# Optimization experiments

Measured on AMD Instinct MI355X. Metric: run time of the kernel, lower is better.

## Reference

```python
import jax, jax.numpy as jnp
import numpy as np

B, N, H, HEADS = 8, 1024, 512, 4  # batch graphs, nodes/graph, graph_hsz, attention heads
R = 64  # relations per graph (passthrough)


def setup_inputs() -> dict:
    key = jax.random.key(0)
    k1, k2, k3, k4, k5, k6, k7 = jax.random.split(key, 7)
    adjs = jax.random.randint(k1, (B, N, N), 0, 2, dtype=jnp.int32)  # 0 => masked
    nodes = jax.random.normal(k2, (B, N, H), dtype=jnp.float32)
    triples = jax.random.normal(k3, (B, R, H), dtype=jnp.float32)   # unused in gat path
    relations = jax.random.normal(k4, (B, R, H), dtype=jnp.float32)  # passthrough
    node_num = jnp.full((B,), N, dtype=jnp.int32)  # all graphs full => no padding branch
    s = 1.0 / np.sqrt(H)
    Wq = (jax.random.normal(k5, (H, H), dtype=jnp.float32) * s)
    Wk = (jax.random.normal(k6, (H, H), dtype=jnp.float32) * s)
    Wv = (jax.random.normal(k7, (H, H), dtype=jnp.float32) * s)
    return {"adjs": adjs, "triples": triples, "nodes": nodes, "node_num": node_num,
            "relations": relations, "Wq": Wq, "Wk": Wk, "Wv": Wv}


def reference(adjs, triples, nodes, node_num, relations, Wq, Wk, Wv):
    b, n, h = nodes.shape
    dk = h // HEADS
    scale = 1.0 / jnp.sqrt(jnp.float32(h))  # torch divides by sqrt(key_dim)=sqrt(H)

    def to_heads(x, W):  # [B,N,H] -> [B,heads,N,dk]; matches split(dim=-1)+stack
        return (x @ W).reshape(b, n, HEADS, dk).transpose(0, 2, 1, 3)

    Q = to_heads(nodes, Wq)
    K = to_heads(nodes, Wk)
    V = to_heads(nodes, Wv)
    att = jnp.einsum('bhnd,bhmd->bhnm', Q, K) * scale
    att = jnp.where((adjs == 0)[:, None, :, :], -jnp.inf, att)
    p = jax.nn.softmax(att, axis=-1)  # dropout_p = blockdrop = 0.0 => identity
    out = jnp.einsum('bhnm,bhmd->bhnd', p, V)
    out = out.transpose(0, 2, 1, 3).reshape(b, n, h)  # concat heads along feature dim
    out = jax.nn.relu(out)
    return (out, relations)
```

## Files before the change

kernel.cpp:

```cpp
#include <hip/hip_runtime.h>
#include <stdint.h>

typedef __attribute__((ext_vector_type(4))) float f32x4;
typedef __attribute__((ext_vector_type(16))) float f32x16;
typedef __attribute__((ext_vector_type(8))) short bf16x8;
typedef __attribute__((ext_vector_type(4))) unsigned uint4v;
typedef unsigned long long ull;

#define GLB_AS const __attribute__((address_space(1)))
#define LDS_AS __attribute__((address_space(3)))

__device__ __forceinline__ short f2bf(float f) {
    union { float f; unsigned u; } x; x.f = f;
    unsigned r = x.u + 0x7FFFu + ((x.u >> 16) & 1u);
    return (short)(r >> 16);
}

__global__ void k_pre(const float* __restrict__ nodes, short* __restrict__ nodes_bf,
                      const float* __restrict__ Wq, const float* __restrict__ Wk,
                      const float* __restrict__ Wv, short* __restrict__ WT,
                      const int* __restrict__ adjs, unsigned* __restrict__ packed) {
    int bi = blockIdx.x, tid = threadIdx.x;
    if (bi < 2048) {
        int i = (bi * 256 + tid) * 8;
        float4 a = *(const float4*)(nodes + i);
        float4 b = *(const float4*)(nodes + i + 4);
        bf16x8 v;
        v[0] = f2bf(a.x); v[1] = f2bf(a.y); v[2] = f2bf(a.z); v[3] = f2bf(a.w);
        v[4] = f2bf(b.x); v[5] = f2bf(b.y); v[6] = f2bf(b.z); v[7] = f2bf(b.w);
        *(bf16x8*)(nodes_bf + i) = v;
    } else if (bi < 5120) {
        int g = (bi - 2048) * 256 + tid;
        int j = g >> 9, k = g & 511;
        int w = j >> 9, n = j & 511;
        const float* W = (w == 0) ? Wq : (w == 1) ? Wk : Wv;
        WT[g] = f2bf(W[k * 512 + n]);
    } else {
        int g = (bi - 5120) * 256 + tid;
        int wv = g >> 6, lane = g & 63;
        ull m = __ballot(adjs[(size_t)wv * 64 + lane] != 0);
        if (lane == 0) *(ull*)(packed + (size_t)wv * 2) = m;
    }
}

__global__ __launch_bounds__(256) void k_gemm_qkv(const short* __restrict__ A,
                                                  const short* __restrict__ WT,
                                                  short* __restrict__ C) {
    __shared__ short Asm[2][128 * 32];
    __shared__ short Bsm[2][128 * 32];
    const int tid = threadIdx.x;
    const int l = tid & 63, w = tid >> 6;
    const int wr = w >> 1, wc = w & 1;
    const int c16 = l & 15, g = l >> 4;
    const int wg = blockIdx.x;
    const int swz = (wg & 7) * 96 + (wg >> 3);
    const int row0 = (swz / 12) * 128, n0 = (swz % 12) * 128;
    f32x4 acc[4][4] = {};

    auto stage = [&](int kt, int bsel) {
        const int k0 = kt * 32;
#pragma unroll
        for (int i = 0; i < 2; ++i) {
            int ch = tid + 256 * i;
            int r = ch >> 2, gc = ch & 3;
            __builtin_amdgcn_global_load_lds((GLB_AS unsigned*)(A + (row0 + r) * 512 + k0 + 8 * gc),
                                             (LDS_AS unsigned*)(&Asm[bsel][ch * 8]), 16, 0, 0);
            __builtin_amdgcn_global_load_lds((GLB_AS unsigned*)(WT + (n0 + r) * 512 + k0 + 8 * gc),
                                             (LDS_AS unsigned*)(&Bsm[bsel][ch * 8]), 16, 0, 0);
        }
    };

    stage(0, 0);
    asm volatile("s_waitcnt vmcnt(0)" ::: "memory");
    __syncthreads();

    for (int kt = 0; kt < 16; ++kt) {
        const int cur = kt & 1;
        if (kt < 15) stage(kt + 1, cur ^ 1);
        bf16x8 af[4], bfr[4];
#pragma unroll
        for (int mf = 0; mf < 4; ++mf)
            af[mf] = *(const bf16x8*)&Asm[cur][(wr * 64 + mf * 16 + c16) * 32 + 8 * g];
#pragma unroll
        for (int nf = 0; nf < 4; ++nf)
            bfr[nf] = *(const bf16x8*)&Bsm[cur][(wc * 64 + nf * 16 + c16) * 32 + 8 * g];
#pragma unroll
        for (int mf = 0; mf < 4; ++mf)
#pragma unroll
            for (int nf = 0; nf < 4; ++nf)
                acc[mf][nf] = __builtin_amdgcn_mfma_f32_16x16x32_bf16(af[mf], bfr[nf], acc[mf][nf], 0, 0, 0);
        asm volatile("s_waitcnt vmcnt(0)" ::: "memory");
        __syncthreads();
    }
#pragma unroll
    for (int mf = 0; mf < 4; ++mf)
#pragma unroll
        for (int nf = 0; nf < 4; ++nf) {
            const float cs = (n0 + wc * 64 + nf * 16 < 512) ? 0.06375872022286384f : 1.0f;
#pragma unroll
            for (int r = 0; r < 4; ++r) {
                int row = row0 + wr * 64 + mf * 16 + 4 * g + r;
                int col = n0 + wc * 64 + nf * 16 + c16;
                C[row * 1536 + col] = f2bf(acc[mf][nf][r] * cs);
            }
        }
}

__global__ __launch_bounds__(256) void k_mid(const short* __restrict__ QKV, short* __restrict__ Vt2,
                                             short* __restrict__ Kt2,
                                             const float* __restrict__ rel_in, float* __restrict__ rel_out) {
    const int bi = blockIdx.x, t = threadIdx.x;
    if (bi >= 1280) {
        int g = (bi - 1280) * 256 + t;
        int c = g & 63, m = (g >> 6) & 1023, b = g >> 16;
        int h = c >> 4, khc = c & 15;
        bf16x8 v = *(const bf16x8*)(QKV + (size_t)(b * 1024 + m) * 1536 + 512 + c * 8);
        *(bf16x8*)(Kt2 + ((((size_t)(b * 4 + h) * 32 + (m >> 5)) * 16 + khc) * 32 + (m & 31)) * 8) = v;
        return;
    }
    if (bi >= 1024) {
        int i = ((bi - 1024) * 256 + t) * 4;
        *(float4*)(rel_out + i) = *(const float4*)(rel_in + i);
        return;
    }
    __shared__ short tile[64 * 65];
    const int b = bi >> 7, n0 = ((bi >> 3) & 15) * 64, d0 = (bi & 7) * 64;
#pragma unroll
    for (int i = 0; i < 16; ++i) {
        int idx = t + 256 * i;
        int nn = idx >> 6, dd = idx & 63;
        tile[nn * 65 + dd] = QKV[(b * 1024 + n0 + nn) * 1536 + 1024 + d0 + dd];
    }
    __syncthreads();
#pragma unroll
    for (int i = 0; i < 2; ++i) {
        int c = t + 256 * i;
        int dd = c >> 3, nl = (c & 7) * 8;
        int dg = d0 + dd;
        int h = dg >> 7, dh = dg & 127;
        bf16x8 v;
#pragma unroll
        for (int e = 0; e < 8; ++e)
            v[e] = tile[(nl + e) * 65 + dd];
        *(bf16x8*)(Vt2 + ((((size_t)(b * 4 + h)) * 128 + ((n0 + nl) >> 3)) * 128 + dh) * 8) = v;
    }
}

__global__ __launch_bounds__(256, 2) void k_attn(const short* __restrict__ QKV, const short* __restrict__ Kt2,
                                                 const short* __restrict__ Vt2,
                                                 const unsigned* __restrict__ packed, float* __restrict__ out) {
    __shared__ char smem[33280];
    float* OshA = (float*)smem;
    float* OshB = (float*)(smem + 16384);
    float* lsh  = (float*)(smem + 32768);
    const int bh = blockIdx.x;
    const int b = bh >> 2, h = bh & 3;
    const int q0 = blockIdx.y * 32;
    const int tid = threadIdx.x, l = tid & 63;
    const int mg = tid >> 6;
    const int l31 = l & 31, hi = l >> 5;

    bf16x8 aq[8];
    const short* Qb = QKV + (size_t)(b * 1024 + q0 + l31) * 1536 + h * 128;
#pragma unroll
    for (int kk = 0; kk < 8; ++kk)
        aq[kk] = *(const bf16x8*)(Qb + kk * 16 + hi * 8);

    f32x16 acc[4] = {};
    float l_lane = 0.f;

    const short* K2b = Kt2 + (size_t)(b * 4 + h) * 131072;
    const short* V2b = Vt2 + (size_t)(b * 4 + h) * 131072;
    const unsigned* adjw = packed + (size_t)(b * 1024 + q0 + l31) * 32 + mg * 8;

    unsigned mall[8];
#pragma unroll
    for (int i = 0; i < 2; ++i)
        *(uint4v*)(mall + 4 * i) = *(const uint4v*)(adjw + 4 * i);

#pragma unroll
    for (int t = 0; t < 8; ++t) {
        const int mt = mg * 8 + t;
        bf16x8 kcur[8], vcur[8];
#pragma unroll
        for (int kk = 0; kk < 8; ++kk)
            kcur[kk] = *(const bf16x8*)(K2b + ((size_t)(mt * 16 + 2 * kk + hi) * 32 + l31) * 8);
        const int mc0 = mg * 32 + t * 4;
#pragma unroll
        for (int ks = 0; ks < 2; ++ks)
#pragma unroll
            for (int dd = 0; dd < 4; ++dd)
                vcur[ks * 4 + dd] = *(const bf16x8*)(V2b + ((size_t)(mc0 + 2 * ks + hi) * 128 + dd * 32 + l31) * 8);

        f32x16 s = (f32x16)0.f;
        __builtin_amdgcn_s_setprio(1);
#pragma unroll
        for (int kk = 0; kk < 8; ++kk)
            s = __builtin_amdgcn_mfma_f32_32x32x16_bf16(kcur[kk], aq[kk], s, 0, 0, 0);
        __builtin_amdgcn_s_setprio(0);

        unsigned pk[4][2];
        const unsigned mshift = mall[t] >> (4 * hi);
        float lt = 0.f;
#pragma unroll
        for (int j = 0; j < 4; ++j) {
            float p[4];
#pragma unroll
            for (int r = 0; r < 4; ++r) {
                float e = __builtin_amdgcn_exp2f(s[4 * j + r]);
                p[r] = ((mshift >> (8 * j + r)) & 1u) ? e : 0.f;
            }
            lt += (p[0] + p[1]) + (p[2] + p[3]);
            asm("v_cvt_pk_bf16_f32 %0, %1, %2" : "=v"(pk[j][0]) : "v"(p[0]), "v"(p[1]));
            asm("v_cvt_pk_bf16_f32 %0, %1, %2" : "=v"(pk[j][1]) : "v"(p[2]), "v"(p[3]));
        }
        l_lane += lt;

        union fragu { unsigned u[4]; bf16x8 v; };
        fragu frag[2];
#pragma unroll
        for (int kh = 0; kh < 2; ++kh) {
            unsigned a0 = pk[2 * kh][0], a1 = pk[2 * kh][1];
            unsigned b0 = pk[2 * kh + 1][0], b1 = pk[2 * kh + 1][1];
            unsigned rx0 = (unsigned)__shfl_xor((int)a0, 32);
            unsigned rx1 = (unsigned)__shfl_xor((int)a1, 32);
            unsigned rx2 = (unsigned)__shfl_xor((int)b0, 32);
            unsigned rx3 = (unsigned)__shfl_xor((int)b1, 32);
            fragu f;
            f.u[0] = hi ? rx2 : a0;
            f.u[1] = hi ? rx3 : a1;
            f.u[2] = hi ? b0 : rx0;
            f.u[3] = hi ? b1 : rx1;
            frag[kh] = f;
        }

        __builtin_amdgcn_s_setprio(1);
#pragma unroll
        for (int ks = 0; ks < 2; ++ks)
#pragma unroll
            for (int dd = 0; dd < 4; ++dd)
                acc[dd] = __builtin_amdgcn_mfma_f32_32x32x16_bf16(frag[ks].v, vcur[ks * 4 + dd], acc[dd], 0, 0, 0);
        __builtin_amdgcn_s_setprio(0);
    }

    l_lane += __shfl_xor(l_lane, 32);
    if (hi == 0) lsh[mg * 32 + l31] = l_lane;

    if (mg == 1 || mg == 3) {
        float* O = (mg == 1) ? OshA : OshB;
#pragma unroll
        for (int dd = 0; dd < 4; ++dd)
#pragma unroll
            for (int j = 0; j < 4; ++j)
#pragma unroll
                for (int r = 0; r < 4; ++r) {
                    int qrow = r + 8 * j + 4 * hi;
                    O[qrow * 128 + dd * 32 + l31] = acc[dd][4 * j + r];
                }
    }
    __syncthreads();
    if (mg == 0 || mg == 2) {
        const float* O = (mg == 0) ? OshA : OshB;
#pragma unroll
        for (int dd = 0; dd < 4; ++dd)
#pragma unroll
            for (int j = 0; j < 4; ++j)
#pragma unroll
                for (int r = 0; r < 4; ++r) {
                    int qrow = r + 8 * j + 4 * hi;
                    acc[dd][4 * j + r] += O[qrow * 128 + dd * 32 + l31];
                }
    }
    __syncthreads();
    if (mg == 2) {
#pragma unroll
        for (int dd = 0; dd < 4; ++dd)
#pragma unroll
            for (int j = 0; j < 4; ++j)
#pragma unroll
                for (int r = 0; r < 4; ++r) {
                    int qrow = r + 8 * j + 4 * hi;
                    OshA[qrow * 128 + dd * 32 + l31] = acc[dd][4 * j + r];
                }
    }
    __syncthreads();
    if (mg == 0) {
        float invq[16];
#pragma unroll
        for (int j = 0; j < 4; ++j)
#pragma unroll
            for (int r = 0; r < 4; ++r) {
                int qrow = r + 8 * j + 4 * hi;
                invq[4 * j + r] = 1.f / (lsh[qrow] + lsh[32 + qrow] + lsh[64 + qrow] + lsh[96 + qrow]);
            }
#pragma unroll
        for (int dd = 0; dd < 4; ++dd)
#pragma unroll
            for (int j = 0; j < 4; ++j)
#pragma unroll
                for (int r = 0; r < 4; ++r) {
                    int qrow = r + 8 * j + 4 * hi;
                    float o = (acc[dd][4 * j + r] + OshA[qrow * 128 + dd * 32 + l31]) * invq[4 * j + r];
                    out[(size_t)(b * 1024 + q0 + qrow) * 512 + h * 128 + dd * 32 + l31] = fmaxf(o, 0.f);
                }
    }
}

extern "C" void kernel_launch(void* const* d_in, const int* in_sizes, int n_in,
                              void* d_out, int out_size, void* d_ws, size_t ws_size,
                              hipStream_t stream) {
    const int*   adjs      = (const int*)d_in[0];
    const float* nodes     = (const float*)d_in[2];
    const float* relations = (const float*)d_in[4];
    const float* Wq        = (const float*)d_in[5];
    const float* Wk        = (const float*)d_in[6];
    const float* Wv        = (const float*)d_in[7];

    char* ws = (char*)d_ws;
    short* nodes_bf   = (short*)(ws);
    short* WT         = (short*)(ws + 8388608);
    short* QKV        = (short*)(ws + 9961472);
    short* Vt2        = (short*)(ws + 35127296);
    unsigned* adjpack = (unsigned*)(ws + 43515904);
    short* Kt2        = (short*)(ws + 44564480);

    float* out     = (float*)d_out;
    float* out_rel = out + 4194304;

    k_pre<<<dim3(37888), dim3(256), 0, stream>>>(nodes, nodes_bf, Wq, Wk, Wv, WT, adjs, adjpack);
    k_gemm_qkv<<<dim3(768), dim3(256), 0, stream>>>(nodes_bf, WT, QKV);
    k_mid<<<dim3(3328), dim3(256), 0, stream>>>(QKV, Vt2, Kt2, relations, out_rel);
    k_attn<<<dim3(32, 32), dim3(256), 0, stream>>>(QKV, Kt2, Vt2, adjpack, out);
}
```

Before: 84.72 us.

## Process two 32-row query tiles per attention block to reuse K/V loads

Each attention block now handles 64 query rows as two 32-row tiles, so every K and V fragment loaded from global memory feeds two MFMAs instead of one. The grid is halved to 512 blocks and LDS grows to about 65KB for the cross-wave reduction buffers. This cuts K/V global traffic per query but doubles accumulator registers (two sets of 4 f32x16). It also halves the block count, which risks lower occupancy, register spills under launch_bounds(256,2), and fewer blocks to fill the GPU.

```diff
diff --git a/kernel.cpp b/kernel.cpp
--- a/kernel.cpp
+++ b/kernel.cpp
@@ -149,160 +149,187 @@
 __global__ __launch_bounds__(256, 2) void k_attn(const short* __restrict__ QKV, const short* __restrict__ Kt2,
                                                  const short* __restrict__ Vt2,
                                                  const unsigned* __restrict__ packed, float* __restrict__ out) {
-    __shared__ char smem[33280];
+    __shared__ char smem[66560];
     float* OshA = (float*)smem;
-    float* OshB = (float*)(smem + 16384);
-    float* lsh  = (float*)(smem + 32768);
+    float* OshB = (float*)(smem + 32768);
+    float* lsh  = (float*)(smem + 65536);
     const int bh = blockIdx.x;
     const int b = bh >> 2, h = bh & 3;
-    const int q0 = blockIdx.y * 32;
+    const int q0 = blockIdx.y * 64;
     const int tid = threadIdx.x, l = tid & 63;
     const int mg = tid >> 6;
     const int l31 = l & 31, hi = l >> 5;
 
-    bf16x8 aq[8];
-    const short* Qb = QKV + (size_t)(b * 1024 + q0 + l31) * 1536 + h * 128;
-#pragma unroll
-    for (int kk = 0; kk < 8; ++kk)
-        aq[kk] = *(const bf16x8*)(Qb + kk * 16 + hi * 8);
-
-    f32x16 acc[4] = {};
-    float l_lane = 0.f;
+    bf16x8 aq[2][8];
+#pragma unroll
+    for (int qt = 0; qt < 2; ++qt) {
+        const short* Qb = QKV + (size_t)(b * 1024 + q0 + qt * 32 + l31) * 1536 + h * 128;
+#pragma unroll
+        for (int kk = 0; kk < 8; ++kk)
+            aq[qt][kk] = *(const bf16x8*)(Qb + kk * 16 + hi * 8);
+    }
+
+    f32x16 acc[2][4] = {};
+    float l_lane[2] = {0.f, 0.f};
 
     const short* K2b = Kt2 + (size_t)(b * 4 + h) * 131072;
     const short* V2b = Vt2 + (size_t)(b * 4 + h) * 131072;
-    const unsigned* adjw = packed + (size_t)(b * 1024 + q0 + l31) * 32 + mg * 8;
-
-    unsigned mall[8];
-#pragma unroll
-    for (int i = 0; i < 2; ++i)
-        *(uint4v*)(mall + 4 * i) = *(const uint4v*)(adjw + 4 * i);
+
+    unsigned mall[2][8];
+#pragma unroll
+    for (int qt = 0; qt < 2; ++qt) {
+        const unsigned* adjw = packed + (size_t)(b * 1024 + q0 + qt * 32 + l31) * 32 + mg * 8;
+#pragma unroll
+        for (int i = 0; i < 2; ++i)
+            *(uint4v*)(&mall[qt][4 * i]) = *(const uint4v*)(adjw + 4 * i);
+    }
 
 #pragma unroll
     for (int t = 0; t < 8; ++t) {
         const int mt = mg * 8 + t;
-        bf16x8 kcur[8], vcur[8];
+        bf16x8 kcur[8];
 #pragma unroll
         for (int kk = 0; kk < 8; ++kk)
             kcur[kk] = *(const bf16x8*)(K2b + ((size_t)(mt * 16 + 2 * kk + hi) * 32 + l31) * 8);
+
+        f32x16 s0 = (f32x16)0.f, s1 = (f32x16)0.f;
+        __builtin_amdgcn_s_setprio(1);
+#pragma unroll
+        for (int kk = 0; kk < 8; ++kk) {
+            s0 = __builtin_amdgcn_mfma_f32_32x32x16_bf16(kcur[kk], aq[0][kk], s0, 0, 0, 0);
+            s1 = __builtin_amdgcn_mfma_f32_32x32x16_bf16(kcur[kk], aq[1][kk], s1, 0, 0, 0);
+        }
+        __builtin_amdgcn_s_setprio(0);
+
+        unsigned pk[2][4][2];
+#pragma unroll
+        for (int qt = 0; qt < 2; ++qt) {
+            const unsigned mshift = mall[qt][t] >> (4 * hi);
+            float lt = 0.f;
+#pragma unroll
+            for (int j = 0; j < 4; ++j) {
+                float p[4];
+#pragma unroll
+                for (int r = 0; r < 4; ++r) {
+                    float e = __builtin_amdgcn_exp2f(qt == 0 ? s0[4 * j + r] : s1[4 * j + r]);
+                    p[r] = ((mshift >> (8 * j + r)) & 1u) ? e : 0.f;
+                }
+                lt += (p[0] + p[1]) + (p[2] + p[3]);
+                asm("v_cvt_pk_bf16_f32 %0, %1, %2" : "=v"(pk[qt][j][0]) : "v"(p[0]), "v"(p[1]));
+                asm("v_cvt_pk_bf16_f32 %0, %1, %2" : "=v"(pk[qt][j][1]) : "v"(p[2]), "v"(p[3]));
+            }
+            l_lane[qt] += lt;
+        }
+
+        union fragu { unsigned u[4]; bf16x8 v; };
+        fragu frag[2][2];
+#pragma unroll
+        for (int qt = 0; qt < 2; ++qt)
+#pragma unroll
+            for (int kh = 0; kh < 2; ++kh) {
+                unsigned a0 = pk[qt][2 * kh][0], a1 = pk[qt][2 * kh][1];
+                unsigned b0 = pk[qt][2 * kh + 1][0], b1 = pk[qt][2 * kh + 1][1];
+                unsigned rx0 = (unsigned)__shfl_xor((int)a0, 32);
+                unsigned rx1 = (unsigned)__shfl_xor((int)a1, 32);
+                unsigned rx2 = (unsigned)__shfl_xor((int)b0, 32);
+                unsigned rx3 = (unsigned)__shfl_xor((int)b1, 32);
+                fragu f;
+                f.u[0] = hi ? rx2 : a0;
+                f.u[1] = hi ? rx3 : a1;
+                f.u[2] = hi ? b0 : rx0;
+                f.u[3] = hi ? b1 : rx1;
+                frag[qt][kh] = f;
+            }
+
         const int mc0 = mg * 32 + t * 4;
 #pragma unroll
-        for (int ks = 0; ks < 2; ++ks)
-#pragma unroll
-            for (int dd = 0; dd < 4; ++dd)
-                vcur[ks * 4 + dd] = *(const bf16x8*)(V2b + ((size_t)(mc0 + 2 * ks + hi) * 128 + dd * 32 + l31) * 8);
-
-        f32x16 s = (f32x16)0.f;
-        __builtin_amdgcn_s_setprio(1);
-#pragma unroll
-        for (int kk = 0; kk < 8; ++kk)
-            s = __builtin_amdgcn_mfma_f32_32x32x16_bf16(kcur[kk], aq[kk], s, 0, 0, 0);
-        __builtin_amdgcn_s_setprio(0);
-
-        unsigned pk[4][2];
-        const unsigned mshift = mall[t] >> (4 * hi);
-        float lt = 0.f;
-#pragma unroll
-        for (int j = 0; j < 4; ++j) {
-            float p[4];
-#pragma unroll
-            for (int r = 0; r < 4; ++r) {
-                float e = __builtin_amdgcn_exp2f(s[4 * j + r]);
-                p[r] = ((mshift >> (8 * j + r)) & 1u) ? e : 0.f;
+        for (int ks = 0; ks < 2; ++ks) {
+            bf16x8 vb[4];
+#pragma unroll
+            for (int dd = 0; dd < 4; ++dd)
+                vb[dd] = *(const bf16x8*)(V2b + ((size_t)(mc0 + 2 * ks + hi) * 128 + dd * 32 + l31) * 8);
+            __builtin_amdgcn_s_setprio(1);
+#pragma unroll
+            for (int dd = 0; dd < 4; ++dd) {
+                acc[0][dd] = __builtin_amdgcn_mfma_f32_32x32x16_bf16(frag[0][ks].v, vb[dd], acc[0][dd], 0, 0, 0);
+                acc[1][dd] = __builtin_amdgcn_mfma_f32_32x32x16_bf16(frag[1][ks].v, vb[dd], acc[1][dd], 0, 0, 0);
             }
-            lt += (p[0] + p[1]) + (p[2] + p[3]);
-            asm("v_cvt_pk_bf16_f32 %0, %1, %2" : "=v"(pk[j][0]) : "v"(p[0]), "v"(p[1]));
-            asm("v_cvt_pk_bf16_f32 %0, %1, %2" : "=v"(pk[j][1]) : "v"(p[2]), "v"(p[3]));
-        }
-        l_lane += lt;
-
-        union fragu { unsigned u[4]; bf16x8 v; };
-        fragu frag[2];
-#pragma unroll
-        for (int kh = 0; kh < 2; ++kh) {
-            unsigned a0 = pk[2 * kh][0], a1 = pk[2 * kh][1];
-            unsigned b0 = pk[2 * kh + 1][0], b1 = pk[2 * kh + 1][1];
-            unsigned rx0 = (unsigned)__shfl_xor((int)a0, 32);
-            unsigned rx1 = (unsigned)__shfl_xor((int)a1, 32);
-            unsigned rx2 = (unsigned)__shfl_xor((int)b0, 32);
-            unsigned rx3 = (unsigned)__shfl_xor((int)b1, 32);
-            fragu f;
-            f.u[0] = hi ? rx2 : a0;
-            f.u[1] = hi ? rx3 : a1;
-            f.u[2] = hi ? b0 : rx0;
-            f.u[3] = hi ? b1 : rx1;
-            frag[kh] = f;
-        }
-
-        __builtin_amdgcn_s_setprio(1);
-#pragma unroll
-        for (int ks = 0; ks < 2; ++ks)
-#pragma unroll
-            for (int dd = 0; dd < 4; ++dd)
-                acc[dd] = __builtin_amdgcn_mfma_f32_32x32x16_bf16(frag[ks].v, vcur[ks * 4 + dd], acc[dd], 0, 0, 0);
-        __builtin_amdgcn_s_setprio(0);
-    }
-
-    l_lane += __shfl_xor(l_lane, 32);
-    if (hi == 0) lsh[mg * 32 + l31] = l_lane;
+            __builtin_amdgcn_s_setprio(0);
+        }
+    }
+
+#pragma unroll
+    for (int qt = 0; qt < 2; ++qt) {
+        l_lane[qt] += __shfl_xor(l_lane[qt], 32);
+        if (hi == 0) lsh[mg * 64 + qt * 32 + l31] = l_lane[qt];
+    }
 
     if (mg == 1 || mg == 3) {
         float* O = (mg == 1) ? OshA : OshB;
 #pragma unroll
-        for (int dd = 0; dd < 4; ++dd)
-#pragma unroll
-            for (int j = 0; j < 4; ++j)
-#pragma unroll
-                for (int r = 0; r < 4; ++r) {
-                    int qrow = r + 8 * j + 4 * hi;
-                    O[qrow * 128 + dd * 32 + l31] = acc[dd][4 * j + r];
-                }
+        for (int qt = 0; qt < 2; ++qt)
+#pragma unroll
+            for (int dd = 0; dd < 4; ++dd)
+#pragma unroll
+                for (int j = 0; j < 4; ++j)
+#pragma unroll
+                    for (int r = 0; r < 4; ++r) {
+                        int qrow = qt * 32 + r + 8 * j + 4 * hi;
+                        O[qrow * 128 + dd * 32 + l31] = acc[qt][dd][4 * j + r];
+                    }
     }
     __syncthreads();
     if (mg == 0 || mg == 2) {
         const float* O = (mg == 0) ? OshA : OshB;
 #pragma unroll
-        for (int dd = 0; dd < 4; ++dd)
+        for (int qt = 0; qt < 2; ++qt)
+#pragma unroll
+            for (int dd = 0; dd < 4; ++dd)
+#pragma unroll
+                for (int j = 0; j < 4; ++j)
+#pragma unroll
+                    for (int r = 0; r < 4; ++r) {
+                        int qrow = qt * 32 + r + 8 * j + 4 * hi;
+                        acc[qt][dd][4 * j + r] += O[qrow * 128 + dd * 32 + l31];
+                    }
+    }
+    __syncthreads();
+    if (mg == 2) {
+#pragma unroll
+        for (int qt = 0; qt < 2; ++qt)
+#pragma unroll
+            for (int dd = 0; dd < 4; ++dd)
+#pragma unroll
+                for (int j = 0; j < 4; ++j)
+#pragma unroll
+                    for (int r = 0; r < 4; ++r) {
+                        int qrow = qt * 32 + r + 8 * j + 4 * hi;
+                        OshA[qrow * 128 + dd * 32 + l31] = acc[qt][dd][4 * j + r];
+                    }
+    }
+    __syncthreads();
+    if (mg == 0) {
+#pragma unroll
+        for (int qt = 0; qt < 2; ++qt) {
+            float invq[16];
 #pragma unroll
             for (int j = 0; j < 4; ++j)
 #pragma unroll
                 for (int r = 0; r < 4; ++r) {
-                    int qrow = r + 8 * j + 4 * hi;
-                    acc[dd][4 * j + r] += O[qrow * 128 + dd * 32 + l31];
+                    int qrow = qt * 32 + r + 8 * j + 4 * hi;
+                    invq[4 * j + r] = 1.f / (lsh[qrow] + lsh[64 + qrow] + lsh[128 + qrow] + lsh[192 + qrow]);
                 }
-    }
-    __syncthreads();
-    if (mg == 2) {
-#pragma unroll
-        for (int dd = 0; dd < 4; ++dd)
-#pragma unroll
-            for (int j = 0; j < 4; ++j)
-#pragma unroll
-                for (int r = 0; r < 4; ++r) {
-                    int qrow = r + 8 * j + 4 * hi;
-                    OshA[qrow * 128 + dd * 32 + l31] = acc[dd][4 * j + r];
-                }
-    }
-    __syncthreads();
-    if (mg == 0) {
-        float invq[16];
-#pragma unroll
-        for (int j = 0; j < 4; ++j)
-#pragma unroll
-            for (int r = 0; r < 4; ++r) {
-                int qrow = r + 8 * j + 4 * hi;
-                invq[4 * j + r] = 1.f / (lsh[qrow] + lsh[32 + qrow] + lsh[64 + qrow] + lsh[96 + qrow]);
-            }
-#pragma unroll
-        for (int dd = 0; dd < 4; ++dd)
-#pragma unroll
-            for (int j = 0; j < 4; ++j)
-#pragma unroll
-                for (int r = 0; r < 4; ++r) {
-                    int qrow = r + 8 * j + 4 * hi;
-                    float o = (acc[dd][4 * j + r] + OshA[qrow * 128 + dd * 32 + l31]) * invq[4 * j + r];
-                    out[(size_t)(b * 1024 + q0 + qrow) * 512 + h * 128 + dd * 32 + l31] = fmaxf(o, 0.f);
-                }
+#pragma unroll
+            for (int dd = 0; dd < 4; ++dd)
+#pragma unroll
+                for (int j = 0; j < 4; ++j)
+#pragma unroll
+                    for (int r = 0; r < 4; ++r) {
+                        int qrow = qt * 32 + r + 8 * j + 4 * hi;
+                        float o = (acc[qt][dd][4 * j + r] + OshA[qrow * 128 + dd * 32 + l31]) * invq[4 * j + r];
+                        out[(size_t)(b * 1024 + q0 + qrow) * 512 + h * 128 + dd * 32 + l31] = fmaxf(o, 0.f);
+                    }
+        }
     }
 }
 
@@ -330,5 +357,5 @@
     k_pre<<<dim3(37888), dim3(256), 0, stream>>>(nodes, nodes_bf, Wq, Wk, Wv, WT, adjs, adjpack);
     k_gemm_qkv<<<dim3(768), dim3(256), 0, stream>>>(nodes_bf, WT, QKV);
     k_mid<<<dim3(3328), dim3(256), 0, stream>>>(QKV, Vt2, Kt2, relations, out_rel);
-    k_attn<<<dim3(32, 32), dim3(256), 0, stream>>>(QKV, Kt2, Vt2, adjpack, out);
-}
+    k_attn<<<dim3(32, 16), dim3(256), 0, stream>>>(QKV, Kt2, Vt2, adjpack, out);
+}
```

New measurement: 164.2 us. +93.8%, slower.
